# Optimization experiments

Measured on AMD Instinct MI355X. Metric: run time of the kernel, lower is better.

Reference implementation:

```python
import jax, jax.numpy as jnp
import numpy as np

N = 172032          # total anchor points (8 images x 21504)
C = 256             # prompt classes
REG_MAX = 16        # DFL bins
M = 64              # GT boxes
IMG = 1024.0
RADIUS = 0.75       # center_sampling_radius
SIGMA = 2.0         # heat sigma
ALPHA, GAMMA = 0.75, 2.0  # varifocal
MARGIN = 8.0
AREA_THR = 0.6
EPS = 1e-6


def setup_inputs() -> dict:
    key = jax.random.key(0)
    ks = jax.random.split(key, 10)
    anchor_points = jax.random.uniform(ks[0], (N, 2)) * IMG
    cls_logits = jax.random.normal(ks[1], (N, C))
    target_scores = jax.random.uniform(ks[2], (N, C))
    pred_dist = jax.random.normal(ks[3], (N, 4, REG_MAX))
    dfl_target = jax.random.uniform(ks[4], (N, 4)) * (REG_MAX - 1)
    # valid xyxy GT boxes inside the image
    xy = jax.random.uniform(ks[5], (M, 2)) * (IMG - 200.0)
    wh = jax.random.uniform(ks[6], (M, 2)) * 180.0 + 20.0
    gt_boxes = jnp.concatenate([xy, xy + wh], axis=-1)
    box_weights = jax.random.uniform(ks[7], (M,))
    pred_boxes = jax.random.uniform(ks[8], (N, 4)) * IMG
    obj_logits = jax.random.normal(ks[9], (N,))
    return {"anchor_points": anchor_points, "cls_logits": cls_logits,
            "target_scores": target_scores, "pred_dist": pred_dist,
            "dfl_target": dfl_target, "gt_boxes": gt_boxes,
            "box_weights": box_weights, "pred_boxes": pred_boxes,
            "obj_logits": obj_logits}


def _inside_and_delta(ap, boxes):
    # ap [N,2], boxes [M,4] -> inside [M,N], delta [M,N,2], half_size [M,1,2]
    inside = ((ap[None, :, 0] >= boxes[:, None, 0]) & (ap[None, :, 0] <= boxes[:, None, 2]) &
              (ap[None, :, 1] >= boxes[:, None, 1]) & (ap[None, :, 1] <= boxes[:, None, 3]))
    center = (boxes[:, :2] + boxes[:, 2:]) * 0.5          # [M,2]
    half = jnp.clip((boxes[:, 2:] - boxes[:, :2]) * 0.5, 1.0)
    delta = (ap[None, :, :] - center[:, None, :]) / half[:, None, :]  # [M,N,2]
    return inside, delta


def build_box_region_weights(ap, boxes, bw, radius):
    inside, delta = _inside_and_delta(ap, boxes)
    center_mask = jnp.max(jnp.abs(delta), axis=-1) <= radius           # [M,N]
    cand = inside & center_mask
    has_cand = jnp.any(cand, axis=1, keepdims=True)
    cand = jnp.where(has_cand, cand, inside)                           # fallback to inside
    return jnp.max(cand.astype(bw.dtype) * bw[:, None], axis=0)        # [N]


def build_center_heat_targets(ap, boxes, sigma):
    sigma = max(float(sigma), 0.001)
    inside, delta = _inside_and_delta(ap, boxes)
    heat = jnp.exp(-0.5 * jnp.sum((delta / sigma) ** 2, axis=-1))      # [M,N]
    heat = heat * inside.astype(heat.dtype)
    return jnp.clip(jnp.max(heat, axis=0), 0.0, 1.0)                   # [N]


def sigmoid_varifocal_loss(logits, targets, alpha, gamma):
    prob = jax.nn.sigmoid(logits)
    weight = alpha * prob ** gamma * (1.0 - targets) + targets
    # stable BCE-with-logits
    bce = jnp.maximum(logits, 0.0) - logits * targets + jnp.log1p(jnp.exp(-jnp.abs(logits)))
    return bce * weight


def dfl_loss(pred_dist, target, reg_max):
    # pred_dist [N,4,R], target [N,4] float in [0, R-1]
    tl = jnp.clip(target.astype(jnp.int32), 0, reg_max - 1)
    tr = jnp.clip(tl + 1, 0, reg_max - 1)
    wl = tr.astype(target.dtype) - target
    wr = 1.0 - wl
    logp = jax.nn.log_softmax(pred_dist, axis=-1)
    ll = -jnp.take_along_axis(logp, tl[..., None], axis=-1)[..., 0]
    lr = -jnp.take_along_axis(logp, tr[..., None], axis=-1)[..., 0]
    return ll * wl + lr * wr                                           # [N,4]


def weighted_mean(loss, weights):
    while weights.ndim < loss.ndim:
        weights = weights[..., None]
    return jnp.sum(loss * weights) / jnp.clip(jnp.sum(weights), EPS)


def oversize_box_penalty(boxes, image_size, area_threshold):
    x1 = jnp.clip(boxes[:, 0], 0.0, image_size)
    y1 = jnp.clip(boxes[:, 1], 0.0, image_size)
    x2 = jnp.clip(boxes[:, 2], 0.0, image_size)
    y2 = jnp.clip(boxes[:, 3], 0.0, image_size)
    w = jnp.clip(x2 - x1, 0.0)
    h = jnp.clip(y2 - y1, 0.0)
    area_ratio = w * h / max(float(image_size * image_size), 1.0)
    edge = ((x1 <= 1.0).astype(boxes.dtype) + (y1 <= 1.0).astype(boxes.dtype) +
            (x2 >= image_size - 1.0).astype(boxes.dtype) + (y2 >= image_size - 1.0).astype(boxes.dtype)) / 4.0
    return jnp.clip(area_ratio - area_threshold, 0.0) * (1.0 + edge)


def reference(anchor_points, cls_logits, target_scores, pred_dist, dfl_target,
              gt_boxes, box_weights, pred_boxes, obj_logits):
    region_w = build_box_region_weights(anchor_points, gt_boxes, box_weights, RADIUS)  # [N]
    heat = build_center_heat_targets(anchor_points, gt_boxes, SIGMA)                   # [N]

    vfl = sigmoid_varifocal_loss(cls_logits, target_scores, ALPHA, GAMMA)              # [N,C]
    cls_loss = weighted_mean(vfl, region_w + heat)

    obj_bce = jnp.maximum(obj_logits, 0.0) - obj_logits * heat + jnp.log1p(jnp.exp(-jnp.abs(obj_logits)))
    obj_loss = jnp.mean(obj_bce)

    dfl = dfl_loss(pred_dist, dfl_target, REG_MAX)                                     # [N,4]
    box_dfl_loss = weighted_mean(dfl, region_w)

    penalty = jnp.mean(oversize_box_penalty(pred_boxes, IMG, AREA_THR))
    margin = jnp.mean(jax.nn.relu(jnp.max(cls_logits, axis=-1) - MARGIN))

    total = cls_loss + obj_loss + box_dfl_loss + 0.1 * penalty + 0.05 * margin
    return total
```

## Files before the change

kernel.cpp:

```cpp
#include <hip/hip_runtime.h>

#define MM 64
#define MAIN_BLOCKS 1344
#define PREP_BLOCKS 672
#define NQ_MAIN 5
#define NQ_PREP 2

__device__ __forceinline__ float vfl1(float l, float t, float* vmax) {
    float e = __expf(-l);
    float p = __fdividef(1.0f, 1.0f + e);
    float q = fmaxf(p, 1.0f - p);
    float bce = fmaf(-l, t, fmaxf(l, 0.0f)) - __logf(q);
    float wgt = fmaf(0.75f * p * p, 1.0f - t, t);
    *vmax = fmaxf(*vmax, l);
    return bce * wgt;
}

__global__ __launch_bounds__(256) void k_hascand(
    const float2* __restrict__ ap, const float4* __restrict__ boxes,
    unsigned long long* __restrict__ mask, int n_pts)
{
    __shared__ float4 sb[MM];
    if (threadIdx.x < MM) sb[threadIdx.x] = boxes[threadIdx.x];
    __syncthreads();
    unsigned long long local = 0ull;
    int stride = gridDim.x * blockDim.x;
    for (int n = blockIdx.x * blockDim.x + threadIdx.x; n < n_pts; n += stride) {
        float2 p = ap[n];
        for (int m = 0; m < MM; ++m) {
            float4 b = sb[m];
            if (p.x >= b.x && p.x <= b.z && p.y >= b.y && p.y <= b.w) {
                float hx = fmaxf((b.z - b.x) * 0.5f, 1.0f);
                float hy = fmaxf((b.w - b.y) * 0.5f, 1.0f);
                float dx = fabsf(p.x - (b.x + b.z) * 0.5f) / hx;
                float dy = fabsf(p.y - (b.y + b.w) * 0.5f) / hy;
                if (fmaxf(dx, dy) <= 0.75f) local |= (1ull << m);
            }
        }
    }
    #pragma unroll
    for (int o = 32; o; o >>= 1) local |= __shfl_xor(local, o);
    if ((threadIdx.x & 63) == 0 && local) atomicOr(mask, local);
}

__global__ __launch_bounds__(256) void k_prep(
    const float2* __restrict__ ap, const float4* __restrict__ boxes,
    const float* __restrict__ bw, const unsigned long long* __restrict__ candmask,
    const float4* __restrict__ pboxes, const float* __restrict__ obj,
    float2* __restrict__ w2, float* __restrict__ prep_partials, int n_pts)
{
    __shared__ float4 sB[MM];
    __shared__ float4 sA[MM];
    __shared__ float  sW[MM];
    if (threadIdx.x < MM) {
        float4 b = boxes[threadIdx.x];
        sB[threadIdx.x] = b;
        float ihx = __fdividef(1.0f, fmaxf((b.z - b.x) * 0.5f, 1.0f));
        float ihy = __fdividef(1.0f, fmaxf((b.w - b.y) * 0.5f, 1.0f));
        sA[threadIdx.x] = make_float4((b.x + b.z) * 0.5f, (b.y + b.w) * 0.5f, ihx, ihy);
        sW[threadIdx.x] = bw[threadIdx.x];
    }
    __syncthreads();
    unsigned long long cm = candmask[0];
    int n = blockIdx.x * blockDim.x + threadIdx.x;
    float aObj = 0.f, aPen = 0.f;
    if (n < n_pts) {
        float2 p = ap[n];
        float rw = 0.f, ht = 0.f;
        #pragma unroll 8
        for (int m = 0; m < MM; ++m) {
            float4 b = sB[m];
            float4 a = sA[m];
            bool inside = (p.x >= b.x) & (p.x <= b.z) & (p.y >= b.y) & (p.y <= b.w);
            float dx = (p.x - a.x) * a.z;
            float dy = (p.y - a.y) * a.w;
            bool cand = inside && (fmaxf(fabsf(dx), fabsf(dy)) <= 0.75f);
            bool eff = ((cm >> m) & 1ull) ? cand : inside;
            if (eff) rw = fmaxf(rw, sW[m]);
            float h = __expf(-0.125f * (dx * dx + dy * dy));
            if (inside) ht = fmaxf(ht, h);
        }
        ht = fminf(ht, 1.0f);
        w2[n] = make_float2(rw + ht, rw);

        float ol = obj[n];
        aObj = fmaxf(ol, 0.f) - ol * ht + __logf(1.0f + __expf(-fabsf(ol)));

        float4 pbx = pboxes[n];
        float x1 = fminf(fmaxf(pbx.x, 0.f), 1024.0f);
        float y1 = fminf(fmaxf(pbx.y, 0.f), 1024.0f);
        float x2 = fminf(fmaxf(pbx.z, 0.f), 1024.0f);
        float y2 = fminf(fmaxf(pbx.w, 0.f), 1024.0f);
        float wq = fmaxf(x2 - x1, 0.f), hq = fmaxf(y2 - y1, 0.f);
        float ar = wq * hq * (1.0f / (1024.0f * 1024.0f));
        float edge = ((x1 <= 1.f ? 1.f : 0.f) + (y1 <= 1.f ? 1.f : 0.f) +
                      (x2 >= 1023.f ? 1.f : 0.f) + (y2 >= 1023.f ? 1.f : 0.f)) * 0.25f;
        aPen = fmaxf(ar - 0.6f, 0.f) * (1.f + edge);
    }
    #pragma unroll
    for (int o = 32; o; o >>= 1) {
        aObj += __shfl_xor(aObj, o);
        aPen += __shfl_xor(aPen, o);
    }
    __shared__ float sh[4][2];
    int lane = threadIdx.x & 63, wid = threadIdx.x >> 6;
    if (lane == 0) { sh[wid][0] = aObj; sh[wid][1] = aPen; }
    __syncthreads();
    if (threadIdx.x < NQ_PREP) {
        prep_partials[blockIdx.x * NQ_PREP + threadIdx.x] =
            sh[0][threadIdx.x] + sh[1][threadIdx.x] + sh[2][threadIdx.x] + sh[3][threadIdx.x];
    }
}

__global__ __launch_bounds__(256) void k_main(
    const float4* __restrict__ cls4,
    const float4* __restrict__ ts4,
    const float*  __restrict__ pd,
    const float*  __restrict__ dflt,
    const float2* __restrict__ w2,
    float* __restrict__ partials,
    int n_pts)
{
    const int tid  = threadIdx.x;
    const int lane = tid & 63;
    const int wid  = tid >> 6;
    const int wave = blockIdx.x * 4 + wid;
    const int CHUNK = MAIN_BLOCKS * 4 * 4;
    const int ksel = lane >> 4;
    const float jjf = (float)(lane & 15);

    float accS1 = 0.f, accS2 = 0.f, accS3 = 0.f, accS4 = 0.f, accMar = 0.f;

    for (int n0 = wave * 4; n0 + 3 < n_pts; n0 += CHUNK) {
        float4 l4[4], t4[4];
        float  xp[4], tg[4];
        float2 wv[4];
        #pragma unroll
        for (int u = 0; u < 4; ++u) {
            int n = n0 + u;
            int o = n * 64 + lane;
            l4[u] = cls4[o];
            t4[u] = ts4[o];
            xp[u] = pd[o];
            wv[u] = w2[n];
            tg[u] = dflt[n * 4 + ksel];
        }
        #pragma unroll
        for (int u = 0; u < 4; ++u) {
            float w = wv[u].x, rw = wv[u].y;
            float vmax = -1e30f;
            float vsum = vfl1(l4[u].x, t4[u].x, &vmax) + vfl1(l4[u].y, t4[u].y, &vmax)
                       + vfl1(l4[u].z, t4[u].z, &vmax) + vfl1(l4[u].w, t4[u].w, &vmax);
            accS1 = fmaf(w, vsum, accS1);
            accS2 += w;
            accS4 += rw;
            if (__any(vmax > 8.0f)) {
                float t = vmax;
                #pragma unroll
                for (int o = 32; o; o >>= 1) t = fmaxf(t, __shfl_xor(t, o));
                accMar += t - 8.0f;
            }
            float e = __expf(xp[u]);
            float se = e;
            #pragma unroll
            for (int o = 8; o; o >>= 1) se += __shfl_xor(se, o);
            float lse = __logf(se);
            float d  = tg[u] - jjf;
            float tw = fmaxf(1.0f - fabsf(d), 0.0f);
            float term = fmaf(-tw, xp[u], lse * 0.0625f);
            accS3 = fmaf(rw, term, accS3);
        }
    }

    #pragma unroll
    for (int o = 32; o; o >>= 1) {
        accS1 += __shfl_xor(accS1, o);
        accS3 += __shfl_xor(accS3, o);
    }
    __shared__ float sh[4][NQ_MAIN];
    if (lane == 0) {
        sh[wid][0] = accS1; sh[wid][1] = accS2; sh[wid][2] = accS3;
        sh[wid][3] = accS4; sh[wid][4] = accMar;
    }
    __syncthreads();
    if (tid < NQ_MAIN) {
        partials[blockIdx.x * NQ_MAIN + tid] =
            sh[0][tid] + sh[1][tid] + sh[2][tid] + sh[3][tid];
    }
}

__global__ __launch_bounds__(256) void k_final(
    const float* __restrict__ mainp, const float* __restrict__ prepp,
    float* __restrict__ out, int n_pts)
{
    double acc[7];
    #pragma unroll
    for (int q = 0; q < 7; ++q) acc[q] = 0.0;
    for (int i = threadIdx.x; i < MAIN_BLOCKS; i += 256) {
        #pragma unroll
        for (int q = 0; q < NQ_MAIN; ++q) acc[q] += (double)mainp[i * NQ_MAIN + q];
    }
    for (int i = threadIdx.x; i < PREP_BLOCKS; i += 256) {
        #pragma unroll
        for (int q = 0; q < NQ_PREP; ++q) acc[5 + q] += (double)prepp[i * NQ_PREP + q];
    }
    __shared__ double sh[256][8];
    #pragma unroll
    for (int q = 0; q < 7; ++q) sh[threadIdx.x][q] = acc[q];
    __syncthreads();
    for (int s = 128; s; s >>= 1) {
        if (threadIdx.x < s) {
            #pragma unroll
            for (int q = 0; q < 7; ++q) sh[threadIdx.x][q] += sh[threadIdx.x + s][q];
        }
        __syncthreads();
    }
    if (threadIdx.x == 0) {
        double S1 = sh[0][0], S2 = sh[0][1], S3 = sh[0][2], S4 = sh[0][3];
        double Sm = sh[0][4], So = sh[0][5], Sp = sh[0][6];
        double invN = 1.0 / (double)n_pts;
        double cls_loss = S1 / fmax(S2, 1e-6);
        double dfl_loss = S3 / fmax(S4, 1e-6);
        out[0] = (float)(cls_loss + So * invN + dfl_loss + 0.1 * Sp * invN + 0.05 * Sm * invN);
    }
}

extern "C" void kernel_launch(void* const* d_in, const int* in_sizes, int n_in,
                              void* d_out, int out_size, void* d_ws, size_t ws_size,
                              hipStream_t stream) {
    const float2* ap    = (const float2*)d_in[0];
    const float4* cls4  = (const float4*)d_in[1];
    const float4* ts4   = (const float4*)d_in[2];
    const float*  pd    = (const float*)d_in[3];
    const float*  dflt  = (const float*)d_in[4];
    const float4* boxes = (const float4*)d_in[5];
    const float*  bw    = (const float*)d_in[6];
    const float4* pbx   = (const float4*)d_in[7];
    const float*  obj   = (const float*)d_in[8];
    int n_pts = in_sizes[0] / 2;

    unsigned long long* mask = (unsigned long long*)d_ws;
    float* main_partials = (float*)((char*)d_ws + 1024);
    float* prep_partials = (float*)((char*)d_ws + 32768);
    float2* w2 = (float2*)((char*)d_ws + 65536);

    hipMemsetAsync(d_ws, 0, 16, stream);
    k_hascand<<<256, 256, 0, stream>>>(ap, boxes, mask, n_pts);
    k_prep<<<PREP_BLOCKS, 256, 0, stream>>>(ap, boxes, bw, mask, pbx, obj, w2,
                                            prep_partials, n_pts);
    k_main<<<MAIN_BLOCKS, 256, 0, stream>>>(cls4, ts4, pd, dflt, w2,
                                            main_partials, n_pts);
    k_final<<<1, 256, 0, stream>>>(main_partials, prep_partials, (float*)d_out, n_pts);
}
```

Before: 144.7 us.

## Restructure main loss kernel: 8-point batches, float4 DFL loads, shuffled weights

The main kernel now gives each wave a contiguous range of 32 anchors, processed as four batches of 8. Each batch issues 16 float4 loads for class logits and targets up front, to keep more memory requests in flight. The DFL logits are read as float4, four bins per lane, so the log-sum-exp needs two shuffles instead of four, and the target weights are computed four at a time. Per-point weights are loaded once per 8 points and spread with lane shuffles. The grid-stride loop is gone, so correctness relies on the launch geometry exactly covering n_pts.

```diff
diff --git a/kernel.cpp b/kernel.cpp
--- a/kernel.cpp
+++ b/kernel.cpp
@@ -115,7 +115,7 @@
 __global__ __launch_bounds__(256) void k_main(
     const float4* __restrict__ cls4,
     const float4* __restrict__ ts4,
-    const float*  __restrict__ pd,
+    const float4* __restrict__ pd4,
     const float*  __restrict__ dflt,
     const float2* __restrict__ w2,
     float* __restrict__ partials,
@@ -125,33 +125,41 @@
     const int lane = tid & 63;
     const int wid  = tid >> 6;
     const int wave = blockIdx.x * 4 + wid;
-    const int CHUNK = MAIN_BLOCKS * 4 * 4;
-    const int ksel = lane >> 4;
-    const float jjf = (float)(lane & 15);
+    const int base = wave * 32;
+
+    const int a_off = lane >> 4;
+    const int r_idx = (lane & 15) >> 2;
+    const float j0  = (float)(4 * (lane & 3));
 
     float accS1 = 0.f, accS2 = 0.f, accS3 = 0.f, accS4 = 0.f, accMar = 0.f;
 
-    for (int n0 = wave * 4; n0 + 3 < n_pts; n0 += CHUNK) {
-        float4 l4[4], t4[4];
-        float  xp[4], tg[4];
-        float2 wv[4];
-        #pragma unroll
-        for (int u = 0; u < 4; ++u) {
-            int n = n0 + u;
-            int o = n * 64 + lane;
-            l4[u] = cls4[o];
-            t4[u] = ts4[o];
-            xp[u] = pd[o];
-            wv[u] = w2[n];
-            tg[u] = dflt[n * 4 + ksel];
-        }
-        #pragma unroll
-        for (int u = 0; u < 4; ++u) {
-            float w = wv[u].x, rw = wv[u].y;
+    #pragma unroll 1
+    for (int blk = 0; blk < 4; ++blk) {
+        const int n0 = base + blk * 8;
+        float4 c4[8], s4[8];
+        #pragma unroll
+        for (int c = 0; c < 8; ++c) {
+            int idx = (n0 + c) * 64 + lane;
+            c4[c] = cls4[idx];
+            s4[c] = ts4[idx];
+        }
+        float4 p4[2];
+        #pragma unroll
+        for (int c = 0; c < 2; ++c) p4[c] = pd4[n0 * 16 + c * 64 + lane];
+        float2 wv = w2[n0 + (lane & 7)];
+        float tgv[2];
+        #pragma unroll
+        for (int c = 0; c < 2; ++c)
+            tgv[c] = dflt[(n0 + c * 4 + a_off) * 4 + r_idx];
+
+        #pragma unroll
+        for (int c = 0; c < 8; ++c) {
+            float w  = __shfl(wv.x, c);
+            float rw = __shfl(wv.y, c);
             float vmax = -1e30f;
-            float vsum = vfl1(l4[u].x, t4[u].x, &vmax) + vfl1(l4[u].y, t4[u].y, &vmax)
-                       + vfl1(l4[u].z, t4[u].z, &vmax) + vfl1(l4[u].w, t4[u].w, &vmax);
-            accS1 = fmaf(w, vsum, accS1);
+            float vs = vfl1(c4[c].x, s4[c].x, &vmax) + vfl1(c4[c].y, s4[c].y, &vmax)
+                     + vfl1(c4[c].z, s4[c].z, &vmax) + vfl1(c4[c].w, s4[c].w, &vmax);
+            accS1 = fmaf(w, vs, accS1);
             accS2 += w;
             accS4 += rw;
             if (__any(vmax > 8.0f)) {
@@ -160,15 +168,23 @@
                 for (int o = 32; o; o >>= 1) t = fmaxf(t, __shfl_xor(t, o));
                 accMar += t - 8.0f;
             }
-            float e = __expf(xp[u]);
-            float se = e;
-            #pragma unroll
-            for (int o = 8; o; o >>= 1) se += __shfl_xor(se, o);
+        }
+
+        #pragma unroll
+        for (int c = 0; c < 2; ++c) {
+            float4 x = p4[c];
+            float se = __expf(x.x) + __expf(x.y) + __expf(x.z) + __expf(x.w);
+            se += __shfl_xor(se, 1);
+            se += __shfl_xor(se, 2);
             float lse = __logf(se);
-            float d  = tg[u] - jjf;
-            float tw = fmaxf(1.0f - fabsf(d), 0.0f);
-            float term = fmaf(-tw, xp[u], lse * 0.0625f);
-            accS3 = fmaf(rw, term, accS3);
+            float tg = tgv[c];
+            float tx = 0.f;
+            tx = fmaf(fmaxf(1.0f - fabsf(tg - j0), 0.f),          x.x, tx);
+            tx = fmaf(fmaxf(1.0f - fabsf(tg - (j0 + 1.f)), 0.f),  x.y, tx);
+            tx = fmaf(fmaxf(1.0f - fabsf(tg - (j0 + 2.f)), 0.f),  x.z, tx);
+            tx = fmaf(fmaxf(1.0f - fabsf(tg - (j0 + 3.f)), 0.f),  x.w, tx);
+            float rwl = __shfl(wv.y, c * 4 + a_off);
+            accS3 = fmaf(rwl, 0.25f * lse - tx, accS3);
         }
     }
 
@@ -231,7 +247,7 @@
     const float2* ap    = (const float2*)d_in[0];
     const float4* cls4  = (const float4*)d_in[1];
     const float4* ts4   = (const float4*)d_in[2];
-    const float*  pd    = (const float*)d_in[3];
+    const float4* pd4   = (const float4*)d_in[3];
     const float*  dflt  = (const float*)d_in[4];
     const float4* boxes = (const float4*)d_in[5];
     const float*  bw    = (const float*)d_in[6];
@@ -248,7 +264,7 @@
     k_hascand<<<256, 256, 0, stream>>>(ap, boxes, mask, n_pts);
     k_prep<<<PREP_BLOCKS, 256, 0, stream>>>(ap, boxes, bw, mask, pbx, obj, w2,
                                             prep_partials, n_pts);
-    k_main<<<MAIN_BLOCKS, 256, 0, stream>>>(cls4, ts4, pd, dflt, w2,
+    k_main<<<MAIN_BLOCKS, 256, 0, stream>>>(cls4, ts4, pd4, dflt, w2,
                                             main_partials, n_pts);
     k_final<<<1, 256, 0, stream>>>(main_partials, prep_partials, (float*)d_out, n_pts);
 }
```

New measurement: 142.8 us. Within noise of the previous version (-1.3%).
